# Kernel optimization log

Measured on AMD Instinct MI355X. Metric: run time of the kernel, lower is better.

Reference implementation:

```python
import jax, jax.numpy as jnp
import numpy as np

B, L, D, H, DH = 2, 2048, 768, 12, 3072
HD = D // H          # head dim = 64
EPS = 1e-6
SCALE = float(np.sqrt(HD))


def setup_inputs() -> dict:
    key = jax.random.key(0)
    ks = jax.random.split(key, 24)
    w = lambda k, shape: jax.random.normal(k, shape, jnp.float32) * 0.02
    # RoPE angles: [L, HD//2]
    inv_freq = 1.0 / (10000.0 ** (jnp.arange(HD // 2, dtype=jnp.float32) / (HD // 2)))
    ang = jnp.arange(L, dtype=jnp.float32)[:, None] * inv_freq[None, :]
    return {
        "x": jax.random.normal(ks[0], (B, L, D), jnp.float32),
        "c": jax.random.normal(ks[1], (B, D), jnp.float32),
        "freqs_cos": jnp.cos(ang),
        "freqs_sin": jnp.sin(ang),
        "W_q": w(ks[2], (D, D)), "W_k": w(ks[3], (D, D)),
        "W_v": w(ks[4], (D, D)), "W_o": w(ks[5], (D, D)),
        "cond_w1": w(ks[6], (D, DH)), "cond_b1": jnp.zeros((DH,), jnp.float32),
        "cond_w2": w(ks[7], (DH, D)), "cond_b2": jnp.zeros((D,), jnp.float32),
        "attn_norm_w": jnp.ones((D,), jnp.float32),
        "attn_alpha": w(ks[8], (D, D)), "attn_beta": w(ks[9], (D, D)),
        "attn_gamma": w(ks[10], (D, D)),
        "ffn_gate": w(ks[11], (D, DH)), "ffn_hidden": w(ks[12], (D, DH)),
        "ffn_out": w(ks[13], (DH, D)),
        "ffn_norm_w": jnp.ones((D,), jnp.float32),
        "ffn_beta": w(ks[14], (D, D)), "ffn_gamma": w(ks[15], (D, D)),
    }


def _rms_norm(x, w):
    return w * x * jax.lax.rsqrt(jnp.mean(x * x, axis=-1, keepdims=True) + EPS)


def _rope(x, cos, sin):
    # x: [b, n, l, hd]; complex pairs are consecutive (even, odd) lanes
    x0, x1 = x[..., 0::2], x[..., 1::2]
    c, s = cos[None, None], sin[None, None]          # [1,1,l,hd//2]
    r0 = x0 * c - x1 * s
    r1 = x0 * s + x1 * c
    return jnp.stack([r0, r1], axis=-1).reshape(x.shape)


def _attention(h, cos, sin, W_q, W_k, W_v, W_o):
    b, l, d = h.shape
    split = lambda y: y.reshape(b, l, H, HD).transpose(0, 2, 1, 3)  # b n l hd
    q = _rope(split(h @ W_q), cos, sin)
    k = _rope(split(h @ W_k), cos, sin)
    v = split(h @ W_v)
    scores = jnp.einsum("bnld,bnmd->bnlm", q, k) / SCALE
    attn = jax.nn.softmax(scores, axis=-1)
    o = jnp.einsum("bnlm,bnmd->bnld", attn, v)
    return o.transpose(0, 2, 1, 3).reshape(b, l, d) @ W_o


def reference(x, c, freqs_cos, freqs_sin, W_q, W_k, W_v, W_o,
              cond_w1, cond_b1, cond_w2, cond_b2,
              attn_norm_w, attn_alpha, attn_beta, attn_gamma,
              ffn_gate, ffn_hidden, ffn_out, ffn_norm_w, ffn_beta, ffn_gamma):
    # conditioning embedding
    c2 = jax.nn.silu(c @ cond_w1 + cond_b1) @ cond_w2 + cond_b2   # [b, d]
    mod = lambda W: (c2 @ W)[:, None]                              # [b, 1, d]
    # attention sub-block with AdaLN modulation + alpha gating
    h = _rms_norm(x, attn_norm_w) * mod(attn_gamma) + mod(attn_beta)
    x = x + _attention(h, freqs_cos, freqs_sin, W_q, W_k, W_v, W_o) * mod(attn_alpha)
    # SwiGLU FFN sub-block (original gates the residual by ffn_gamma, not alpha)
    h = _rms_norm(x, ffn_norm_w) * mod(ffn_gamma) + mod(ffn_beta)
    ff = (jax.nn.silu(h @ ffn_gate) * (h @ ffn_hidden)) @ ffn_out
    return x + ff * mod(ffn_gamma)
```

## Files before the change

kernel.cpp:

```cpp
#include <hip/hip_runtime.h>

typedef unsigned short u16;
typedef __attribute__((ext_vector_type(8))) short short8;
typedef __attribute__((ext_vector_type(4))) float f32x4;

#define L_SEQ 2048
#define NHEAD 12
#define KVB 128

__device__ __forceinline__ u16 f2bf(float f) {
    union { float f; unsigned u; } x; x.f = f;
    unsigned r = x.u + 0x7fffu + ((x.u >> 16) & 1u);
    return (u16)(r >> 16);
}
__device__ __forceinline__ float bf2f(u16 u) {
    union { unsigned u; float f; } x; x.u = ((unsigned)u) << 16;
    return x.f;
}
__device__ __forceinline__ float silu_f(float x) { return x / (1.f + __expf(-x)); }

__device__ __forceinline__ void gload16(const u16* g, u16* l) {
    __builtin_amdgcn_global_load_lds(
        (const __attribute__((address_space(1))) void*)g,
        (__attribute__((address_space(3))) void*)l, 16, 0, 0);
}

__global__ __launch_bounds__(256) void transpose_convert4(
    const float* __restrict__ S0, const float* __restrict__ S1,
    const float* __restrict__ S2, const float* __restrict__ S3,
    u16* __restrict__ D0, u16* __restrict__ D1, u16* __restrict__ D2, u16* __restrict__ D3,
    int K, int N)
{
    const float* W = (blockIdx.z == 0) ? S0 : (blockIdx.z == 1) ? S1 : (blockIdx.z == 2) ? S2 : S3;
    u16* Wt = (blockIdx.z == 0) ? D0 : (blockIdx.z == 1) ? D1 : (blockIdx.z == 2) ? D2 : D3;
    __shared__ float t[32][33];
    int tx = threadIdx.x & 31, ty = threadIdx.x >> 5;
    int n0 = blockIdx.x * 32, k0 = blockIdx.y * 32;
#pragma unroll
    for (int i = 0; i < 4; i++)
        t[ty + 8 * i][tx] = W[(size_t)(k0 + ty + 8 * i) * N + n0 + tx];
    __syncthreads();
#pragma unroll
    for (int i = 0; i < 4; i++)
        Wt[(size_t)(n0 + ty + 8 * i) * K + k0 + tx] = f2bf(t[tx][ty + 8 * i]);
}

__global__ __launch_bounds__(256) void cond_mlp1(
    const float* __restrict__ c, const float* __restrict__ w1, float* __restrict__ part)
{
    int j = blockIdx.x * 256 + threadIdx.x;
    int d0 = blockIdx.y * 96;
    float a0 = 0.f, a1 = 0.f;
    for (int d = d0; d < d0 + 96; ++d) {
        float w = w1[(size_t)d * 3072 + j];
        a0 += c[d] * w;
        a1 += c[768 + d] * w;
    }
    part[(size_t)(blockIdx.y * 2 + 0) * 3072 + j] = a0;
    part[(size_t)(blockIdx.y * 2 + 1) * 3072 + j] = a1;
}

__global__ __launch_bounds__(256) void cond_mlp2(
    const float* __restrict__ part, const float* __restrict__ b1,
    const float* __restrict__ w2, float* __restrict__ c2part)
{
    __shared__ float hid[2][384];
    const int tid = threadIdx.x;
    const int d0 = blockIdx.y * 384;
    for (int i = tid; i < 768; i += 256) {
        int b = i / 384, dd = i - b * 384;
        float s = b1[d0 + dd];
#pragma unroll
        for (int p = 0; p < 8; p++) s += part[(size_t)(p * 2 + b) * 3072 + d0 + dd];
        hid[b][dd] = silu_f(s);
    }
    __syncthreads();
    int jj = tid & 63, kc = tid >> 6;
    int j = blockIdx.x * 64 + jj;
    float a0 = 0.f, a1 = 0.f;
    for (int dd = kc * 96; dd < kc * 96 + 96; ++dd) {
        float w = w2[(size_t)(d0 + dd) * 768 + j];
        a0 += hid[0][dd] * w;
        a1 += hid[1][dd] * w;
    }
    __shared__ float r0[256], r1[256];
    r0[tid] = a0; r1[tid] = a1;
    __syncthreads();
    if (kc == 0) {
        a0 = r0[jj] + r0[64 + jj] + r0[128 + jj] + r0[192 + jj];
        a1 = r1[jj] + r1[64 + jj] + r1[128 + jj] + r1[192 + jj];
        c2part[(size_t)(blockIdx.y * 2 + 0) * 768 + j] = a0;
        c2part[(size_t)(blockIdx.y * 2 + 1) * 768 + j] = a1;
    }
}

__global__ __launch_bounds__(256) void mod_gemm(
    const float* __restrict__ c2part, const float* __restrict__ b2,
    const float* __restrict__ W0, const float* __restrict__ W1,
    const float* __restrict__ W2, const float* __restrict__ W3,
    const float* __restrict__ W4, float* __restrict__ out)
{
    __shared__ float c2s[2][768];
    const int tid = threadIdx.x;
    for (int i = tid; i < 1536; i += 256) {
        int b = i / 768, d = i - b * 768;
        float s = b2[d];
#pragma unroll
        for (int p = 0; p < 8; p++) s += c2part[(size_t)(p * 2 + b) * 768 + d];
        c2s[b][d] = s;
    }
    __syncthreads();
    int w = blockIdx.y;
    const float* W = (w == 0) ? W0 : (w == 1) ? W1 : (w == 2) ? W2 : (w == 3) ? W3 : W4;
    int jj = tid & 63, kc = tid >> 6;
    int j = blockIdx.x * 64 + jj;
    float a0 = 0.f, a1 = 0.f;
    for (int d = kc * 192; d < kc * 192 + 192; ++d) {
        float ww = W[(size_t)d * 768 + j];
        a0 += c2s[0][d] * ww;
        a1 += c2s[1][d] * ww;
    }
    __shared__ float r0[256], r1[256];
    r0[tid] = a0; r1[tid] = a1;
    __syncthreads();
    if (kc == 0) {
        a0 = r0[jj] + r0[64 + jj] + r0[128 + jj] + r0[192 + jj];
        a1 = r1[jj] + r1[64 + jj] + r1[128 + jj] + r1[192 + jj];
        out[(size_t)(w * 2 + 0) * 768 + j] = a0;
        out[(size_t)(w * 2 + 1) * 768 + j] = a1;
    }
}

__global__ __launch_bounds__(256) void rmsnorm_mod(
    const float* __restrict__ xin, const float* __restrict__ nw,
    const float* __restrict__ gamma, const float* __restrict__ beta,
    u16* __restrict__ hout)
{
    int row = blockIdx.x;
    int b = row >> 11;
    const float* xr = xin + (size_t)row * 768;
    int t = threadIdx.x;
    float v0 = xr[t], v1 = xr[t + 256], v2 = xr[t + 512];
    float ss = v0 * v0 + v1 * v1 + v2 * v2;
#pragma unroll
    for (int m = 1; m < 64; m <<= 1) ss += __shfl_xor(ss, m);
    __shared__ float red[4];
    if ((t & 63) == 0) red[t >> 6] = ss;
    __syncthreads();
    float tot = red[0] + red[1] + red[2] + red[3];
    float rr = rsqrtf(tot * (1.f / 768.f) + 1e-6f);
    u16* ho = hout + (size_t)row * 768;
    const float* g = gamma + (size_t)b * 768;
    const float* be = beta + (size_t)b * 768;
#pragma unroll
    for (int i = 0; i < 3; i++) {
        int col = t + i * 256;
        float v = (i == 0) ? v0 : (i == 1) ? v1 : v2;
        ho[col] = f2bf(v * rr * nw[col] * g[col] + be[col]);
    }
}

template<int BM, int WM, int MODE>
__global__ __launch_bounds__(256) void gemm_bf16(
    const u16* __restrict__ A, const u16* __restrict__ Bt,
    float* __restrict__ Cf, u16* __restrict__ Cb,
    const float* __restrict__ X, const float* __restrict__ coef,
    int M, int N, int K)
{
    constexpr int MR = WM / 16, NR = 4;
    __shared__ __align__(16) u16 As[2][BM * 32];
    __shared__ __align__(16) u16 Bs[2][128 * 32];
    const int tid = threadIdx.x;
    const int lane = tid & 63, wid = tid >> 6;
    const int lo = lane & 15, hi = lane >> 4;
    const int bm = blockIdx.x * BM, bn = blockIdx.y * 128;
    const int wrow = (wid >> 1) * WM, wcol = (wid & 1) * 64;

    f32x4 acc[MR][NR];
#pragma unroll
    for (int a = 0; a < MR; a++)
#pragma unroll
        for (int b = 0; b < NR; b++)
            acc[a][b] = (f32x4){0.f, 0.f, 0.f, 0.f};

    auto stage = [&](int buf, int k0) {
#pragma unroll
        for (int p = 0; p < BM / 64; p++) {
            int ch = tid + p * 256;
            gload16(A + (size_t)(bm + (ch >> 2)) * K + k0 + (ch & 3) * 8, &As[buf][ch * 8]);
        }
#pragma unroll
        for (int p = 0; p < 2; p++) {
            int ch = tid + p * 256;
            gload16(Bt + (size_t)(bn + (ch >> 2)) * K + k0 + (ch & 3) * 8, &Bs[buf][ch * 8]);
        }
    };

    stage(0, 0);
    int cur = 0;
    const int NT = K >> 5;
    for (int t = 0; t < NT; t++) {
        __syncthreads();
        if (t + 1 < NT) stage(cur ^ 1, (t + 1) * 32);
        short8 af[MR], bfr[NR];
#pragma unroll
        for (int mi = 0; mi < MR; mi++)
            af[mi] = *(const short8*)(&As[cur][(wrow + mi * 16 + lo) * 32 + hi * 8]);
#pragma unroll
        for (int nj = 0; nj < NR; nj++)
            bfr[nj] = *(const short8*)(&Bs[cur][(wcol + nj * 16 + lo) * 32 + hi * 8]);
        __builtin_amdgcn_s_setprio(1);
#pragma unroll
        for (int mi = 0; mi < MR; mi++)
#pragma unroll
            for (int nj = 0; nj < NR; nj++)
                acc[mi][nj] = __builtin_amdgcn_mfma_f32_16x16x32_bf16(af[mi], bfr[nj], acc[mi][nj], 0, 0, 0);
        __builtin_amdgcn_s_setprio(0);
        cur ^= 1;
    }
#pragma unroll
    for (int mi = 0; mi < MR; mi++)
#pragma unroll
        for (int nj = 0; nj < NR; nj++)
#pragma unroll
            for (int i = 0; i < 4; i++) {
                int row = bm + wrow + mi * 16 + hi * 4 + i;
                int col = bn + wcol + nj * 16 + lo;
                size_t idx = (size_t)row * N + col;
                float v = acc[mi][nj][i];
                if (MODE == 1) {
                    Cb[idx] = f2bf(v);
                } else {
                    int b = row >> 11;
                    Cf[idx] = X[idx] + v * coef[(size_t)b * N + col];
                }
            }
}

__global__ __launch_bounds__(256) void gemm_ffn1(
    const u16* __restrict__ A, const u16* __restrict__ Gt, const u16* __restrict__ Ht,
    u16* __restrict__ ff, int M, int N, int K)
{
    __shared__ __align__(16) u16 As[2][128 * 32];
    __shared__ __align__(16) u16 Gs[2][64 * 32];
    __shared__ __align__(16) u16 Hs[2][64 * 32];
    const int tid = threadIdx.x;
    const int lane = tid & 63, wid = tid >> 6;
    const int lo = lane & 15, hi = lane >> 4;
    const int bm = blockIdx.x * 128, bn = blockIdx.y * 64;
    const int wrow = (wid >> 1) * 64, wcol = (wid & 1) * 32;

    f32x4 ag[4][2], ah[4][2];
#pragma unroll
    for (int a = 0; a < 4; a++)
#pragma unroll
        for (int b = 0; b < 2; b++) {
            ag[a][b] = (f32x4){0.f, 0.f, 0.f, 0.f};
            ah[a][b] = (f32x4){0.f, 0.f, 0.f, 0.f};
        }

    auto stage = [&](int buf, int k0) {
#pragma unroll
        for (int p = 0; p < 2; p++) {
            int ch = tid + p * 256;
            gload16(A + (size_t)(bm + (ch >> 2)) * K + k0 + (ch & 3) * 8, &As[buf][ch * 8]);
        }
        {
            int ch = tid;
            gload16(Gt + (size_t)(bn + (ch >> 2)) * K + k0 + (ch & 3) * 8, &Gs[buf][ch * 8]);
            gload16(Ht + (size_t)(bn + (ch >> 2)) * K + k0 + (ch & 3) * 8, &Hs[buf][ch * 8]);
        }
    };

    stage(0, 0);
    int cur = 0;
    const int NT = K >> 5;
    for (int t = 0; t < NT; t++) {
        __syncthreads();
        if (t + 1 < NT) stage(cur ^ 1, (t + 1) * 32);
        short8 af[4], gf[2], hf[2];
#pragma unroll
        for (int mi = 0; mi < 4; mi++)
            af[mi] = *(const short8*)(&As[cur][(wrow + mi * 16 + lo) * 32 + hi * 8]);
#pragma unroll
        for (int nj = 0; nj < 2; nj++) {
            gf[nj] = *(const short8*)(&Gs[cur][(wcol + nj * 16 + lo) * 32 + hi * 8]);
            hf[nj] = *(const short8*)(&Hs[cur][(wcol + nj * 16 + lo) * 32 + hi * 8]);
        }
        __builtin_amdgcn_s_setprio(1);
#pragma unroll
        for (int mi = 0; mi < 4; mi++)
#pragma unroll
            for (int nj = 0; nj < 2; nj++) {
                ag[mi][nj] = __builtin_amdgcn_mfma_f32_16x16x32_bf16(af[mi], gf[nj], ag[mi][nj], 0, 0, 0);
                ah[mi][nj] = __builtin_amdgcn_mfma_f32_16x16x32_bf16(af[mi], hf[nj], ah[mi][nj], 0, 0, 0);
            }
        __builtin_amdgcn_s_setprio(0);
        cur ^= 1;
    }
#pragma unroll
    for (int mi = 0; mi < 4; mi++)
#pragma unroll
        for (int nj = 0; nj < 2; nj++)
#pragma unroll
            for (int i = 0; i < 4; i++) {
                int row = bm + wrow + mi * 16 + hi * 4 + i;
                int col = bn + wcol + nj * 16 + lo;
                ff[(size_t)row * N + col] = f2bf(silu_f(ag[mi][nj][i]) * ah[mi][nj][i]);
            }
}

__global__ __launch_bounds__(256) void rope_reshape(
    const u16* __restrict__ qr, const u16* __restrict__ kr, const u16* __restrict__ vr,
    const float* __restrict__ fc, const float* __restrict__ fs,
    u16* __restrict__ qo, u16* __restrict__ ko, u16* __restrict__ vt)
{
    const float QSCALE = 0.125f * 1.44269504f;
    __shared__ u16 Vl[64 * 64];
    const int tid = threadIdx.x;
    const int bh = blockIdx.y, lt = blockIdx.x;
    const int b = bh / NHEAD, h = bh % NHEAD;
    const int l0 = lt * 64;
    const int lrow = tid >> 2, ch = tid & 3;

    const size_t srow = ((size_t)(b * L_SEQ + l0 + lrow)) * 2304 + h * 64 + ch * 16;
    const size_t drow = ((size_t)(bh * L_SEQ + l0 + lrow)) * 64 + ch * 16;

    float cs[8], sn[8];
#pragma unroll
    for (int i = 0; i < 8; i++) {
        cs[i] = fc[(l0 + lrow) * 32 + ch * 8 + i];
        sn[i] = fs[(l0 + lrow) * 32 + ch * 8 + i];
    }
    union { int4 v4[2]; u16 s[16]; } iv, ov;
    iv.v4[0] = *(const int4*)(qr + srow); iv.v4[1] = *(const int4*)(qr + srow + 8);
#pragma unroll
    for (int i = 0; i < 8; i++) {
        float x0 = bf2f(iv.s[2 * i]), x1 = bf2f(iv.s[2 * i + 1]);
        ov.s[2 * i]     = f2bf((x0 * cs[i] - x1 * sn[i]) * QSCALE);
        ov.s[2 * i + 1] = f2bf((x0 * sn[i] + x1 * cs[i]) * QSCALE);
    }
    *(int4*)(qo + drow) = ov.v4[0]; *(int4*)(qo + drow + 8) = ov.v4[1];
    iv.v4[0] = *(const int4*)(kr + srow); iv.v4[1] = *(const int4*)(kr + srow + 8);
#pragma unroll
    for (int i = 0; i < 8; i++) {
        float x0 = bf2f(iv.s[2 * i]), x1 = bf2f(iv.s[2 * i + 1]);
        ov.s[2 * i]     = f2bf(x0 * cs[i] - x1 * sn[i]);
        ov.s[2 * i + 1] = f2bf(x0 * sn[i] + x1 * cs[i]);
    }
    *(int4*)(ko + drow) = ov.v4[0]; *(int4*)(ko + drow + 8) = ov.v4[1];
    iv.v4[0] = *(const int4*)(vr + srow); iv.v4[1] = *(const int4*)(vr + srow + 8);
#pragma unroll
    for (int e = 0; e < 16; e++) {
        int d = ch * 16 + e;
        Vl[d * 64 + (lrow ^ (((d >> 3) & 7) << 3))] = iv.s[e];
    }
    __syncthreads();
    const int d = tid >> 2;
    const int key = ((d >> 3) & 7) << 3;
    int4 o0 = *(const int4*)(&Vl[d * 64 + ((ch * 16) ^ key)]);
    int4 o1 = *(const int4*)(&Vl[d * 64 + ((ch * 16 + 8) ^ key)]);
    u16* vd = vt + ((size_t)bh * 64 + d) * L_SEQ + l0 + ch * 16;
    *(int4*)(vd) = o0; *(int4*)(vd + 8) = o1;
}

__global__ __launch_bounds__(256) void attn_fwd(
    const u16* __restrict__ q, const u16* __restrict__ k, const u16* __restrict__ vt,
    u16* __restrict__ outp)
{
    __shared__ __align__(16) u16 Kb[2][KVB * 64];
    __shared__ __align__(16) u16 Vb[2][64 * KVB];
    __shared__ __align__(16) u16 Ps[4][16 * KVB];
    const int tid = threadIdx.x;
    const int lane = tid & 63, wid = tid >> 6;
    const int lo = lane & 15, hi = lane >> 4;
    const int qt = blockIdx.x, bh = blockIdx.y;
    const int b = bh / NHEAD, h = bh % NHEAD;
    const int q0 = qt * 64 + wid * 16;
    const u16* qb = q + ((size_t)bh * L_SEQ + q0) * 64;
    const u16* kbase = k + (size_t)bh * L_SEQ * 64;
    const u16* vbase = vt + (size_t)bh * 64 * L_SEQ;

    short8 qa0 = *(const short8*)(qb + lo * 64 + hi * 8);
    short8 qa1 = *(const short8*)(qb + lo * 64 + 32 + hi * 8);

    f32x4 oacc[4];
#pragma unroll
    for (int dt = 0; dt < 4; dt++) oacc[dt] = (f32x4){0.f, 0.f, 0.f, 0.f};
    float m_ = -1e30f, ls = 0.f;

    auto stage = [&](int buf, int kv0) {
#pragma unroll
        for (int p = 0; p < 4; p++) {
            int chk = tid + p * 256;
            int r = chk >> 3;
            int sl = (chk & 7) ^ (r & 7);
            gload16(kbase + (size_t)(kv0 + r) * 64 + sl * 8, &Kb[buf][chk * 8]);
        }
#pragma unroll
        for (int p = 0; p < 4; p++) {
            int chk = tid + p * 256;
            int r = chk >> 4;
            int cc = (chk & 15) ^ (r & 7);
            gload16(vbase + (size_t)r * L_SEQ + kv0 + cc * 8, &Vb[buf][chk * 8]);
        }
    };

    stage(0, 0);
    int cur = 0;
    u16* pw = &Ps[wid][0];
    const int pkey = (lo & 7) << 3;
    for (int t = 0; t < L_SEQ / KVB; t++) {
        __syncthreads();
        if (t + 1 < L_SEQ / KVB) stage(cur ^ 1, (t + 1) * KVB);
        f32x4 s[8];
#pragma unroll
        for (int nt = 0; nt < 8; nt++) {
            int kr = nt * 16 + lo;
            const u16* kp = &Kb[cur][kr * 64];
            int key = (kr & 7) << 3;
            short8 kf0 = *(const short8*)(kp + ((hi * 8) ^ key));
            short8 kf1 = *(const short8*)(kp + ((32 + hi * 8) ^ key));
            __builtin_amdgcn_s_setprio(1);
            f32x4 z = (f32x4){0.f, 0.f, 0.f, 0.f};
            z = __builtin_amdgcn_mfma_f32_16x16x32_bf16(kf0, qa0, z, 0, 0, 0);
            s[nt] = __builtin_amdgcn_mfma_f32_16x16x32_bf16(kf1, qa1, s[nt] = z, 0, 0, 0);
            __builtin_amdgcn_s_setprio(0);
        }
        float pmax = -1e30f;
#pragma unroll
        for (int nt = 0; nt < 8; nt++) {
            float tn = fmaxf(fmaxf(s[nt][0], s[nt][1]), fmaxf(s[nt][2], s[nt][3]));
            pmax = fmaxf(pmax, tn);
        }
        pmax = fmaxf(pmax, __shfl_xor(pmax, 16));
        pmax = fmaxf(pmax, __shfl_xor(pmax, 32));
        if (!__all(pmax - m_ <= 8.f)) {
            float mn = fmaxf(m_, pmax);
            float al = exp2f(m_ - mn);
            m_ = mn;
            ls *= al;
#pragma unroll
            for (int dt = 0; dt < 4; dt++) oacc[dt] *= al;
        }
        float rs = 0.f;
#pragma unroll
        for (int nt = 0; nt < 8; nt++)
#pragma unroll
            for (int r = 0; r < 4; r++) {
                float p = exp2f(s[nt][r] - m_);
                s[nt][r] = p;
                rs += p;
            }
        rs += __shfl_xor(rs, 16);
        rs += __shfl_xor(rs, 32);
        ls += rs;
#pragma unroll
        for (int nt = 0; nt < 8; nt++) {
            unsigned w0, w1;
            asm("v_cvt_pk_bf16_f32 %0, %1, %2" : "=v"(w0) : "v"(s[nt][0]), "v"(s[nt][1]));
            asm("v_cvt_pk_bf16_f32 %0, %1, %2" : "=v"(w1) : "v"(s[nt][2]), "v"(s[nt][3]));
            uint2 pk2; pk2.x = w0; pk2.y = w1;
            *(uint2*)(pw + lo * KVB + ((nt * 16 + hi * 4) ^ pkey)) = pk2;
        }
        short8 pa[4];
#pragma unroll
        for (int kk = 0; kk < 4; kk++)
            pa[kk] = *(const short8*)(pw + lo * KVB + ((kk * 32 + hi * 8) ^ pkey));
#pragma unroll
        for (int dt = 0; dt < 4; dt++) {
            int vr_ = dt * 16 + lo;
            const u16* vp = &Vb[cur][vr_ * KVB];
            int vkey = (vr_ & 7) << 3;
            __builtin_amdgcn_s_setprio(1);
#pragma unroll
            for (int kk = 0; kk < 4; kk++) {
                short8 vf = *(const short8*)(vp + ((kk * 32 + hi * 8) ^ vkey));
                oacc[dt] = __builtin_amdgcn_mfma_f32_16x16x32_bf16(vf, pa[kk], oacc[dt], 0, 0, 0);
            }
            __builtin_amdgcn_s_setprio(0);
        }
        cur ^= 1;
    }
    float inv = 1.f / ls;
    int qrow = q0 + lo;
    u16* orow = outp + ((size_t)(b * L_SEQ + qrow)) * 768 + h * 64;
#pragma unroll
    for (int dt = 0; dt < 4; dt++)
#pragma unroll
        for (int r = 0; r < 4; r++)
            orow[dt * 16 + hi * 4 + r] = f2bf(oacc[dt][r] * inv);
}

extern "C" void kernel_launch(void* const* d_in, const int* in_sizes, int n_in,
                              void* d_out, int out_size, void* d_ws, size_t ws_size,
                              hipStream_t stream)
{
    const float* x      = (const float*)d_in[0];
    const float* c      = (const float*)d_in[1];
    const float* fcos   = (const float*)d_in[2];
    const float* fsin   = (const float*)d_in[3];
    const float* Wq     = (const float*)d_in[4];
    const float* Wk     = (const float*)d_in[5];
    const float* Wv     = (const float*)d_in[6];
    const float* Wo     = (const float*)d_in[7];
    const float* cw1    = (const float*)d_in[8];
    const float* cb1    = (const float*)d_in[9];
    const float* cw2    = (const float*)d_in[10];
    const float* cb2    = (const float*)d_in[11];
    const float* anw    = (const float*)d_in[12];
    const float* Walpha = (const float*)d_in[13];
    const float* Wbeta  = (const float*)d_in[14];
    const float* Wgamma = (const float*)d_in[15];
    const float* Wgate  = (const float*)d_in[16];
    const float* Whid   = (const float*)d_in[17];
    const float* Wout   = (const float*)d_in[18];
    const float* fnw    = (const float*)d_in[19];
    const float* Wbetaf = (const float*)d_in[20];
    const float* Wgammaf= (const float*)d_in[21];

    const int M = 4096;
    char* ws = (char*)d_ws;
    size_t off = 0;
    auto alloc = [&](size_t bytes) -> char* {
        char* p = ws + off;
        off += (bytes + 255) & ~(size_t)255;
        return p;
    };
    u16* wq_t   = (u16*)alloc((size_t)768 * 768 * 2);
    u16* wk_t   = (u16*)alloc((size_t)768 * 768 * 2);
    u16* wv_t   = (u16*)alloc((size_t)768 * 768 * 2);
    u16* wo_t   = (u16*)alloc((size_t)768 * 768 * 2);
    u16* gate_t = (u16*)alloc((size_t)3072 * 768 * 2);
    u16* hid_t  = (u16*)alloc((size_t)3072 * 768 * 2);
    u16* out_t  = (u16*)alloc((size_t)768 * 3072 * 2);
    float* part1 = (float*)alloc((size_t)8 * 2 * 3072 * 4);
    float* part2 = (float*)alloc((size_t)8 * 2 * 768 * 4);
    float* mods = (float*)alloc(5 * 2 * 768 * 4);
    u16* hbuf   = (u16*)alloc((size_t)M * 768 * 2);
    u16* qkvraw = (u16*)alloc((size_t)M * 2304 * 2);
    u16* qrope  = (u16*)alloc((size_t)M * 768 * 2);
    u16* krope  = (u16*)alloc((size_t)M * 768 * 2);
    u16* vtb    = (u16*)alloc((size_t)M * 768 * 2);
    u16* attnh  = (u16*)alloc((size_t)M * 768 * 2);
    float* ybuf = (float*)alloc((size_t)M * 768 * 4);
    u16* ffbuf  = (u16*)alloc((size_t)M * 3072 * 2);

    transpose_convert4<<<dim3(24, 24, 4), 256, 0, stream>>>(
        Wq, Wk, Wv, Wo, wq_t, wk_t, wv_t, wo_t, 768, 768);
    transpose_convert4<<<dim3(96, 24, 2), 256, 0, stream>>>(
        Wgate, Whid, Wgate, Whid, gate_t, hid_t, gate_t, hid_t, 768, 3072);
    transpose_convert4<<<dim3(24, 96, 1), 256, 0, stream>>>(
        Wout, Wout, Wout, Wout, out_t, out_t, out_t, out_t, 3072, 768);

    cond_mlp1<<<dim3(12, 8), 256, 0, stream>>>(c, cw1, part1);
    cond_mlp2<<<dim3(12, 8), 256, 0, stream>>>(part1, cb1, cw2, part2);
    mod_gemm<<<dim3(12, 5), 256, 0, stream>>>(
        part2, cb2, Wgamma, Wbeta, Walpha, Wgammaf, Wbetaf, mods);

    rmsnorm_mod<<<M, 256, 0, stream>>>(x, anw, mods + 0 * 1536, mods + 1 * 1536, hbuf);

    gemm_bf16<128, 64, 1><<<dim3(32, 18, 1), 256, 0, stream>>>(
        hbuf, wq_t, nullptr, qkvraw, nullptr, nullptr, M, 2304, 768);

    rope_reshape<<<dim3(32, 24), 256, 0, stream>>>(
        qkvraw, qkvraw + 768, qkvraw + 1536,
        fcos, fsin, qrope, krope, vtb);

    attn_fwd<<<dim3(32, 24), 256, 0, stream>>>(qrope, krope, vtb, attnh);

    gemm_bf16<64, 32, 2><<<dim3(64, 6, 1), 256, 0, stream>>>(
        attnh, wo_t, ybuf, nullptr, x, mods + 2 * 1536, M, 768, 768);

    rmsnorm_mod<<<M, 256, 0, stream>>>(ybuf, fnw, mods + 3 * 1536, mods + 4 * 1536, hbuf);

    gemm_ffn1<<<dim3(32, 48), 256, 0, stream>>>(
        hbuf, gate_t, hid_t, ffbuf, M, 3072, 768);

    gemm_bf16<64, 32, 2><<<dim3(64, 6, 1), 256, 0, stream>>>(
        ffbuf, out_t, (float*)d_out, nullptr, ybuf, mods + 3 * 1536, M, 768, 3072);
}
```

Before: 298.6 us.

## Stage attention K/V through registers, remap blocks per XCD, pack output stores

The attention kernel stops using double-buffered direct global-to-LDS loads. It now prefetches the next K/V tile into registers and writes them to a single LDS buffer between two barriers, which halves K/V LDS usage and may raise occupancy. The V swizzle widens to 16 groups, the P swizzle key uses all of lo, and the grid becomes 1D with a mapping that puts three heads on each XCD to improve L2 reuse of K/V. Output is written as packed bf16 pairs. The trade is an extra barrier per tile and more registers held across the loop.

```diff
diff --git a/kernel.cpp b/kernel.cpp
--- a/kernel.cpp
+++ b/kernel.cpp
@@ -368,13 +368,16 @@
     const u16* __restrict__ q, const u16* __restrict__ k, const u16* __restrict__ vt,
     u16* __restrict__ outp)
 {
-    __shared__ __align__(16) u16 Kb[2][KVB * 64];
-    __shared__ __align__(16) u16 Vb[2][64 * KVB];
+    __shared__ __align__(16) u16 Kb[KVB * 64];
+    __shared__ __align__(16) u16 Vb[64 * KVB];
     __shared__ __align__(16) u16 Ps[4][16 * KVB];
     const int tid = threadIdx.x;
     const int lane = tid & 63, wid = tid >> 6;
     const int lo = lane & 15, hi = lane >> 4;
-    const int qt = blockIdx.x, bh = blockIdx.y;
+    const int lid = blockIdx.x;
+    const int xcd = lid & 7, li = lid >> 3;
+    const int bh = xcd * 3 + (li >> 5);
+    const int qt = li & 31;
     const int b = bh / NHEAD, h = bh % NHEAD;
     const int q0 = qt * 64 + wid * 16;
     const u16* qb = q + ((size_t)bh * L_SEQ + q0) * 64;
@@ -389,35 +392,44 @@
     for (int dt = 0; dt < 4; dt++) oacc[dt] = (f32x4){0.f, 0.f, 0.f, 0.f};
     float m_ = -1e30f, ls = 0.f;
 
-    auto stage = [&](int buf, int kv0) {
+    int4 kreg[4], vreg[4];
+    auto load_regs = [&](int kv0) {
 #pragma unroll
         for (int p = 0; p < 4; p++) {
-            int chk = tid + p * 256;
-            int r = chk >> 3;
-            int sl = (chk & 7) ^ (r & 7);
-            gload16(kbase + (size_t)(kv0 + r) * 64 + sl * 8, &Kb[buf][chk * 8]);
+            int ch = tid + p * 256;
+            int r = ch >> 3, g = ch & 7;
+            kreg[p] = *(const int4*)(kbase + (size_t)(kv0 + r) * 64 + (g ^ (r & 7)) * 8);
         }
 #pragma unroll
         for (int p = 0; p < 4; p++) {
-            int chk = tid + p * 256;
-            int r = chk >> 4;
-            int cc = (chk & 15) ^ (r & 7);
-            gload16(vbase + (size_t)r * L_SEQ + kv0 + cc * 8, &Vb[buf][chk * 8]);
+            int ch = tid + p * 256;
+            int r = ch >> 4, g = ch & 15;
+            vreg[p] = *(const int4*)(vbase + (size_t)r * L_SEQ + kv0 + (g ^ (r & 15)) * 8);
         }
     };
-
-    stage(0, 0);
-    int cur = 0;
+    auto write_lds = [&]() {
+#pragma unroll
+        for (int p = 0; p < 4; p++)
+            *(int4*)(&Kb[(tid + p * 256) * 8]) = kreg[p];
+#pragma unroll
+        for (int p = 0; p < 4; p++)
+            *(int4*)(&Vb[(tid + p * 256) * 8]) = vreg[p];
+    };
+
+    load_regs(0);
+    const int NT = L_SEQ / KVB;
     u16* pw = &Ps[wid][0];
-    const int pkey = (lo & 7) << 3;
-    for (int t = 0; t < L_SEQ / KVB; t++) {
+    const int pkey = lo << 3;
+    for (int t = 0; t < NT; t++) {
         __syncthreads();
-        if (t + 1 < L_SEQ / KVB) stage(cur ^ 1, (t + 1) * KVB);
+        write_lds();
+        if (t + 1 < NT) load_regs((t + 1) * KVB);
+        __syncthreads();
         f32x4 s[8];
 #pragma unroll
         for (int nt = 0; nt < 8; nt++) {
             int kr = nt * 16 + lo;
-            const u16* kp = &Kb[cur][kr * 64];
+            const u16* kp = &Kb[kr * 64];
             int key = (kr & 7) << 3;
             short8 kf0 = *(const short8*)(kp + ((hi * 8) ^ key));
             short8 kf1 = *(const short8*)(kp + ((32 + hi * 8) ^ key));
@@ -470,8 +482,8 @@
 #pragma unroll
         for (int dt = 0; dt < 4; dt++) {
             int vr_ = dt * 16 + lo;
-            const u16* vp = &Vb[cur][vr_ * KVB];
-            int vkey = (vr_ & 7) << 3;
+            const u16* vp = &Vb[vr_ * KVB];
+            int vkey = (vr_ & 15) << 3;
             __builtin_amdgcn_s_setprio(1);
 #pragma unroll
             for (int kk = 0; kk < 4; kk++) {
@@ -480,16 +492,20 @@
             }
             __builtin_amdgcn_s_setprio(0);
         }
-        cur ^= 1;
     }
     float inv = 1.f / ls;
     int qrow = q0 + lo;
     u16* orow = outp + ((size_t)(b * L_SEQ + qrow)) * 768 + h * 64;
 #pragma unroll
-    for (int dt = 0; dt < 4; dt++)
-#pragma unroll
-        for (int r = 0; r < 4; r++)
-            orow[dt * 16 + hi * 4 + r] = f2bf(oacc[dt][r] * inv);
+    for (int dt = 0; dt < 4; dt++) {
+        unsigned w0, w1;
+        float o0 = oacc[dt][0] * inv, o1 = oacc[dt][1] * inv;
+        float o2 = oacc[dt][2] * inv, o3 = oacc[dt][3] * inv;
+        asm("v_cvt_pk_bf16_f32 %0, %1, %2" : "=v"(w0) : "v"(o0), "v"(o1));
+        asm("v_cvt_pk_bf16_f32 %0, %1, %2" : "=v"(w1) : "v"(o2), "v"(o3));
+        uint2 pk2; pk2.x = w0; pk2.y = w1;
+        *(uint2*)(orow + dt * 16 + hi * 4) = pk2;
+    }
 }
 
 extern "C" void kernel_launch(void* const* d_in, const int* in_sizes, int n_in,
@@ -567,7 +583,7 @@
         qkvraw, qkvraw + 768, qkvraw + 1536,
         fcos, fsin, qrope, krope, vtb);
 
-    attn_fwd<<<dim3(32, 24), 256, 0, stream>>>(qrope, krope, vtb, attnh);
+    attn_fwd<<<dim3(768), 256, 0, stream>>>(qrope, krope, vtb, attnh);
 
     gemm_bf16<64, 32, 2><<<dim3(64, 6, 1), 256, 0, stream>>>(
         attnh, wo_t, ybuf, nullptr, x, mods + 2 * 1536, M, 768, 768);
```

Result: slower. 330.6 us (+10.7%).
